# Optimization experiments

Measured on AMD Instinct MI355X. Metric: run time of the kernel, lower is better.

## Reference

```python
import jax, jax.numpy as jnp
import numpy as np

F_DIM = 64

def setup_inputs() -> dict:
    key = jax.random.key(0)
    ks = jax.random.split(key, 10)
    E, N, C, M, H, D = 1600000, 50000, 3, 7, 32, 64
    gamma = 10.0
    inp = {
        'edge_attr': jax.random.normal(ks[0], (E, D), jnp.float32),
        'node_coords': jax.random.normal(ks[1], (N, C), jnp.float32),
        'edge_index': jax.random.randint(ks[2], (2, E), 0, N, jnp.int64),
        'Wr': jax.random.normal(ks[3], (F_DIM // 2, M), jnp.float32) * (gamma ** -2),
        'W1': jax.random.normal(ks[4], (H, F_DIM), jnp.float32) * (1.0 / np.sqrt(F_DIM)),
        'b1': jax.random.normal(ks[5], (H,), jnp.float32) * 0.02,
        'W2': jax.random.normal(ks[6], (D, H), jnp.float32) * (1.0 / np.sqrt(H)),
        'b2': jax.random.normal(ks[7], (D,), jnp.float32) * 0.02,
        'Wf': jax.random.normal(ks[8], (D, D), jnp.float32) * (1.0 / np.sqrt(D)),
        'bf': jax.random.normal(ks[9], (D,), jnp.float32) * 0.02,
    }
    return inp

def reference(edge_attr, node_coords, edge_index, Wr, W1, b1, W2, b2, Wf, bf):
    u, v = edge_index[0], edge_index[1]
    Cu = node_coords[u]                      # (E, 3) gather
    Cv = node_coords[v]
    delta = Cv - Cu
    mid = 0.5 * (Cu + Cv)
    length = jnp.linalg.norm(delta, axis=-1, keepdims=True)
    geom = jnp.concatenate([delta, mid, length], axis=-1)   # (E, 7)
    # Learnable Fourier PE (G=1): proj -> [cos|sin]/sqrt(F) -> GELU MLP
    proj = geom @ Wr.T                                      # (E, F/2)
    fourier = jnp.concatenate([jnp.cos(proj), jnp.sin(proj)], axis=-1) / jnp.sqrt(jnp.float32(F_DIM))
    h = jax.nn.gelu(fourier @ W1.T + b1, approximate=False)
    pe = h @ W2.T + b2                                      # (E, D)
    # fuse == 'add'
    return edge_attr + (pe @ Wf.T + bf)
```

## Files before the change

### kernel.cpp

```cpp
#include <hip/hip_runtime.h>
#include <math.h>

#define EPB 256

typedef float f32x2 __attribute__((ext_vector_type(2)));
typedef float f32x4 __attribute__((ext_vector_type(4)));

__global__ void lfpe_precompute(const float* __restrict__ W2,
                                const float* __restrict__ b2,
                                const float* __restrict__ Wf,
                                const float* __restrict__ bf,
                                const int* __restrict__ eidx32,
                                float* __restrict__ ws) {
    const int t = threadIdx.x;
    for (int idx = t; idx < 2048; idx += 256) {
        const int j = idx >> 6, d = idx & 63;
        float s = 0.f;
        #pragma unroll 8
        for (int k = 0; k < 64; ++k) s += Wf[d * 64 + k] * W2[k * 32 + j];
        ws[j * 64 + d] = s;
    }
    if (t < 64) {
        float s = bf[t];
        #pragma unroll 8
        for (int k = 0; k < 64; ++k) s += Wf[t * 64 + k] * b2[k];
        ws[2048 + t] = s;
    }
    __shared__ int nz;
    if (t == 0) nz = 0;
    __syncthreads();
    if (t < 64 && eidx32[2 * t + 1] != 0) atomicAdd(&nz, 1);
    __syncthreads();
    if (t == 0) ((int*)ws)[2112] = (nz == 0) ? 1 : 0;
}

__global__ __launch_bounds__(256) void lfpe_main(
    const float* __restrict__ edge_attr,
    const float* __restrict__ coords,
    const void*  __restrict__ eidx,
    const float* __restrict__ Wr,
    const float* __restrict__ W1,
    const float* __restrict__ b1,
    const float* __restrict__ ws,
    float* __restrict__ out,
    const int E)
{
    __shared__ float sWr[32 * 8];
    __shared__ float sW1p[32 * 64];
    __shared__ float sb1[32];
    __shared__ f32x4 sh4[8 * EPB];

    const int tid = threadIdx.x;

    for (int idx = tid; idx < 2048; idx += 256) {
        const int i = idx >> 6, r = idx & 63;
        sW1p[idx] = W1[(r >> 1) * 64 + (r & 1) * 32 + i];
    }
    {
        const int i = tid >> 3, m = tid & 7;
        sWr[tid] = (m < 7) ? Wr[i * 7 + m] : 0.f;
    }
    if (tid < 32) sb1[tid] = b1[tid];

    const int is64 = ((const int*)ws)[2112];
    const int e = blockIdx.x * EPB + tid;

    float acc[32];
    #pragma unroll
    for (int j = 0; j < 32; ++j) acc[j] = 0.f;

    __syncthreads();

    if (e < E) {
        long long u, v;
        if (is64) {
            u = ((const long long*)eidx)[e];
            v = ((const long long*)eidx)[E + e];
        } else {
            u = ((const int*)eidx)[e];
            v = ((const int*)eidx)[E + e];
        }
        const float* cu = coords + 3 * (int)u;
        const float* cv = coords + 3 * (int)v;
        const float ux = cu[0], uy = cu[1], uz = cu[2];
        const float vx = cv[0], vy = cv[1], vz = cv[2];
        float g[7];
        g[0] = vx - ux; g[1] = vy - uy; g[2] = vz - uz;
        g[3] = 0.5f * (ux + vx); g[4] = 0.5f * (uy + vy); g[5] = 0.5f * (uz + vz);
        g[6] = sqrtf(g[0] * g[0] + g[1] * g[1] + g[2] * g[2]);

        #pragma unroll 4
        for (int i = 0; i < 32; ++i) {
            float p = 0.f;
            #pragma unroll
            for (int m = 0; m < 7; ++m) p += g[m] * sWr[i * 8 + m];
            const float c = __cosf(p);
            const float s = __sinf(p);
            const f32x4* wrow = (const f32x4*)&sW1p[i * 64];
            #pragma unroll
            for (int j4 = 0; j4 < 16; ++j4) {
                const f32x4 w = wrow[j4];
                acc[j4 * 2 + 0] += c * w.x + s * w.y;
                acc[j4 * 2 + 1] += c * w.z + s * w.w;
            }
        }
        #pragma unroll
        for (int j = 0; j < 32; ++j) {
            const float hp = acc[j] * 0.125f + sb1[j];
            acc[j] = 0.5f * hp * (1.f + erff(hp * 0.70710678118654752f));
        }
    }

    #pragma unroll
    for (int j4 = 0; j4 < 8; ++j4) {
        f32x4 hv;
        hv.x = acc[4 * j4]; hv.y = acc[4 * j4 + 1];
        hv.z = acc[4 * j4 + 2]; hv.w = acc[4 * j4 + 3];
        sh4[j4 * EPB + tid] = hv;
    }

    __syncthreads();

    const int d2  = (tid & 31) * 2;
    const int sub = tid >> 5;
    float w2a[32], w2b[32];
    #pragma unroll
    for (int j = 0; j < 32; ++j) {
        const f32x2 wp = *(const f32x2*)&ws[j * 64 + d2];
        w2a[j] = wp.x; w2b[j] = wp.y;
    }
    const f32x2 bb = *(const f32x2*)&ws[2048 + d2];

    const long long base = (long long)blockIdx.x * EPB;
    const float* ea = edge_attr + base * 64 + sub * 64 + d2;
    float*       op = out       + base * 64 + sub * 64 + d2;

    #pragma unroll 4
    for (int it = 0; it < 32; ++it) {
        const int el = it * 8 + sub;
        if (base + el < E) {
            const f32x2 av = __builtin_nontemporal_load((const f32x2*)(ea + it * 512));
            float a = bb.x, b = bb.y;
            #pragma unroll
            for (int j4 = 0; j4 < 8; ++j4) {
                const f32x4 hv = sh4[j4 * EPB + el];
                a += hv.x * w2a[4 * j4]     + hv.y * w2a[4 * j4 + 1] +
                     hv.z * w2a[4 * j4 + 2] + hv.w * w2a[4 * j4 + 3];
                b += hv.x * w2b[4 * j4]     + hv.y * w2b[4 * j4 + 1] +
                     hv.z * w2b[4 * j4 + 2] + hv.w * w2b[4 * j4 + 3];
            }
            f32x2 r; r.x = av.x + a; r.y = av.y + b;
            __builtin_nontemporal_store(r, (f32x2*)(op + it * 512));
        }
    }
}

extern "C" void kernel_launch(void* const* d_in, const int* in_sizes, int n_in,
                              void* d_out, int out_size, void* d_ws, size_t ws_size,
                              hipStream_t stream) {
    const float* edge_attr = (const float*)d_in[0];
    const float* coords    = (const float*)d_in[1];
    const void*  eidx      = (const void*) d_in[2];
    const float* Wr        = (const float*)d_in[3];
    const float* W1        = (const float*)d_in[4];
    const float* b1        = (const float*)d_in[5];
    const float* W2        = (const float*)d_in[6];
    const float* b2        = (const float*)d_in[7];
    const float* Wf        = (const float*)d_in[8];
    const float* bf        = (const float*)d_in[9];
    float* out = (float*)d_out;
    float* ws  = (float*)d_ws;

    const int E = in_sizes[2] / 2;

    hipLaunchKernelGGL(lfpe_precompute, dim3(1), dim3(256), 0, stream,
                       W2, b2, Wf, bf, (const int*)eidx, ws);

    const int nblk = (E + EPB - 1) / EPB;
    hipLaunchKernelGGL(lfpe_main, dim3(nblk), dim3(256), 0, stream,
                       edge_attr, coords, eidx, Wr, W1, b1, ws, out, E);
}
```

Baseline: 1.017 ms.

## Use fp16 packed dot products for both MLP matmuls with fp32 accumulation

Both small matmuls now run on packed fp16 pairs through the fdot2 instruction, with fp32 accumulation. The cos/sin features and W1 are packed as half2 for the first layer. The GELU hidden activations and the fused W2·Wf weights are packed as half2 for the second layer. This roughly halves the FMA instruction count, the shared-memory footprint and traffic, and the register use for the weights. The price is fp16 rounding of the weights, the features and the hidden activations, which may loosen accuracy.

After: 891.2 us. 12.4% less time.

```diff
diff --git a/kernel.cpp b/kernel.cpp
--- a/kernel.cpp
+++ b/kernel.cpp
@@ -5,6 +5,18 @@
 
 typedef float f32x2 __attribute__((ext_vector_type(2)));
 typedef float f32x4 __attribute__((ext_vector_type(4)));
+typedef _Float16 f16x2 __attribute__((ext_vector_type(2)));
+
+__device__ inline f16x2 as_h2(float f) { union { float f; f16x2 h; } u; u.f = f; return u.h; }
+__device__ inline float as_f32(f16x2 h) { union { float f; f16x2 h; } u; u.h = h; return u.f; }
+
+__device__ inline float fdot2f(f16x2 a, f16x2 b, float c) {
+#if __has_builtin(__builtin_amdgcn_fdot2)
+    return __builtin_amdgcn_fdot2(a, b, c, false);
+#else
+    return c + (float)a.x * (float)b.x + (float)a.y * (float)b.y;
+#endif
+}
 
 __global__ void lfpe_precompute(const float* __restrict__ W2,
                                 const float* __restrict__ b2,
@@ -13,25 +25,30 @@
                                 const int* __restrict__ eidx32,
                                 float* __restrict__ ws) {
     const int t = threadIdx.x;
-    for (int idx = t; idx < 2048; idx += 256) {
-        const int j = idx >> 6, d = idx & 63;
-        float s = 0.f;
+    for (int idx = t; idx < 1024; idx += 256) {
+        const int jp = idx >> 6, d = idx & 63;
+        float s0 = 0.f, s1 = 0.f;
         #pragma unroll 8
-        for (int k = 0; k < 64; ++k) s += Wf[d * 64 + k] * W2[k * 32 + j];
-        ws[j * 64 + d] = s;
+        for (int k = 0; k < 64; ++k) {
+            const float w = Wf[d * 64 + k];
+            s0 += w * W2[k * 32 + 2 * jp];
+            s1 += w * W2[k * 32 + 2 * jp + 1];
+        }
+        f16x2 p; p.x = (_Float16)s0; p.y = (_Float16)s1;
+        ws[idx] = as_f32(p);
     }
     if (t < 64) {
         float s = bf[t];
         #pragma unroll 8
         for (int k = 0; k < 64; ++k) s += Wf[t * 64 + k] * b2[k];
-        ws[2048 + t] = s;
+        ws[1024 + t] = s;
     }
     __shared__ int nz;
     if (t == 0) nz = 0;
     __syncthreads();
     if (t < 64 && eidx32[2 * t + 1] != 0) atomicAdd(&nz, 1);
     __syncthreads();
-    if (t == 0) ((int*)ws)[2112] = (nz == 0) ? 1 : 0;
+    if (t == 0) ((int*)ws)[1100] = (nz == 0) ? 1 : 0;
 }
 
 __global__ __launch_bounds__(256) void lfpe_main(
@@ -46,15 +63,18 @@
     const int E)
 {
     __shared__ float sWr[32 * 8];
-    __shared__ float sW1p[32 * 64];
+    __shared__ float sW1h[32 * 32];
     __shared__ float sb1[32];
-    __shared__ f32x4 sh4[8 * EPB];
+    __shared__ f32x4 sh2[4 * EPB];
 
     const int tid = threadIdx.x;
 
-    for (int idx = tid; idx < 2048; idx += 256) {
-        const int i = idx >> 6, r = idx & 63;
-        sW1p[idx] = W1[(r >> 1) * 64 + (r & 1) * 32 + i];
+    for (int idx = tid; idx < 1024; idx += 256) {
+        const int i = idx >> 5, j = idx & 31;
+        f16x2 p;
+        p.x = (_Float16)W1[j * 64 + i];
+        p.y = (_Float16)W1[j * 64 + 32 + i];
+        sW1h[idx] = as_f32(p);
     }
     {
         const int i = tid >> 3, m = tid & 7;
@@ -62,7 +82,7 @@
     }
     if (tid < 32) sb1[tid] = b1[tid];
 
-    const int is64 = ((const int*)ws)[2112];
+    const int is64 = ((const int*)ws)[1100];
     const int e = blockIdx.x * EPB + tid;
 
     float acc[32];
@@ -94,14 +114,17 @@
             float p = 0.f;
             #pragma unroll
             for (int m = 0; m < 7; ++m) p += g[m] * sWr[i * 8 + m];
-            const float c = __cosf(p);
-            const float s = __sinf(p);
-            const f32x4* wrow = (const f32x4*)&sW1p[i * 64];
+            f16x2 cs;
+            cs.x = (_Float16)__cosf(p);
+            cs.y = (_Float16)__sinf(p);
+            const f32x4* wrow = (const f32x4*)&sW1h[i * 32];
             #pragma unroll
-            for (int j4 = 0; j4 < 16; ++j4) {
-                const f32x4 w = wrow[j4];
-                acc[j4 * 2 + 0] += c * w.x + s * w.y;
-                acc[j4 * 2 + 1] += c * w.z + s * w.w;
+            for (int r = 0; r < 8; ++r) {
+                const f32x4 w = wrow[r];
+                acc[r * 4 + 0] = fdot2f(cs, as_h2(w.x), acc[r * 4 + 0]);
+                acc[r * 4 + 1] = fdot2f(cs, as_h2(w.y), acc[r * 4 + 1]);
+                acc[r * 4 + 2] = fdot2f(cs, as_h2(w.z), acc[r * 4 + 2]);
+                acc[r * 4 + 3] = fdot2f(cs, as_h2(w.w), acc[r * 4 + 3]);
             }
         }
         #pragma unroll
@@ -112,24 +135,30 @@
     }
 
     #pragma unroll
-    for (int j4 = 0; j4 < 8; ++j4) {
-        f32x4 hv;
-        hv.x = acc[4 * j4]; hv.y = acc[4 * j4 + 1];
-        hv.z = acc[4 * j4 + 2]; hv.w = acc[4 * j4 + 3];
-        sh4[j4 * EPB + tid] = hv;
-    }
-
-    __syncthreads();
+    for (int c = 0; c < 4; ++c) {
+        f32x4 ch;
+        #pragma unroll
+        for (int q = 0; q < 4; ++q) {
+            const int jp = c * 4 + q;
+            f16x2 hh;
+            hh.x = (_Float16)acc[2 * jp];
+            hh.y = (_Float16)acc[2 * jp + 1];
+            ch[q] = as_f32(hh);
+        }
+        sh2[c * EPB + tid] = ch;
+    }
 
     const int d2  = (tid & 31) * 2;
     const int sub = tid >> 5;
-    float w2a[32], w2b[32];
+    f16x2 wA[16], wB[16];
     #pragma unroll
-    for (int j = 0; j < 32; ++j) {
-        const f32x2 wp = *(const f32x2*)&ws[j * 64 + d2];
-        w2a[j] = wp.x; w2b[j] = wp.y;
-    }
-    const f32x2 bb = *(const f32x2*)&ws[2048 + d2];
+    for (int jp = 0; jp < 16; ++jp) {
+        wA[jp] = as_h2(ws[jp * 64 + d2]);
+        wB[jp] = as_h2(ws[jp * 64 + d2 + 1]);
+    }
+    const f32x2 bb = *(const f32x2*)&ws[1024 + d2];
+
+    __syncthreads();
 
     const long long base = (long long)blockIdx.x * EPB;
     const float* ea = edge_attr + base * 64 + sub * 64 + d2;
@@ -142,12 +171,15 @@
             const f32x2 av = __builtin_nontemporal_load((const f32x2*)(ea + it * 512));
             float a = bb.x, b = bb.y;
             #pragma unroll
-            for (int j4 = 0; j4 < 8; ++j4) {
-                const f32x4 hv = sh4[j4 * EPB + el];
-                a += hv.x * w2a[4 * j4]     + hv.y * w2a[4 * j4 + 1] +
-                     hv.z * w2a[4 * j4 + 2] + hv.w * w2a[4 * j4 + 3];
-                b += hv.x * w2b[4 * j4]     + hv.y * w2b[4 * j4 + 1] +
-                     hv.z * w2b[4 * j4 + 2] + hv.w * w2b[4 * j4 + 3];
+            for (int c = 0; c < 4; ++c) {
+                const f32x4 hv = sh2[c * EPB + el];
+                #pragma unroll
+                for (int q = 0; q < 4; ++q) {
+                    const int jp = c * 4 + q;
+                    const f16x2 hq = as_h2(hv[q]);
+                    a = fdot2f(hq, wA[jp], a);
+                    b = fdot2f(hq, wB[jp], b);
+                }
             }
             f32x2 r; r.x = av.x + a; r.y = av.y + b;
             __builtin_nontemporal_store(r, (f32x2*)(op + it * 512));
```
